# Kernel tuning notes

Hardware: AMD Instinct MI355X
Metric: run time of the kernel (lower is better)

The kernel has to match this reference:

```python
import jax, jax.numpy as jnp
import numpy as np

N_SITES = 64   # lattice sites
BOND = 32      # virtual bond dimension D
PHYS = 2       # physical (spin) dimension
BATCH = 32768  # Monte Carlo samples


def spin_to_occupancy(s):
    # spins in {-1,+1} -> physical indices in {0,1}
    return ((s + 1) // 2).astype(jnp.int32)


def setup_inputs() -> dict:
    key = jax.random.key(0)
    k1, k2, k3, k4 = jax.random.split(key, 4)
    # site tensors: boundary sites have bond dim 1, interior sites are (PHYS, D, D)
    t_first = jax.random.uniform(k1, (PHYS, 1, BOND), dtype=jnp.float32)
    t_mid = jax.random.uniform(k2, (N_SITES - 2, PHYS, BOND, BOND), dtype=jnp.float32)
    t_last = jax.random.uniform(k3, (PHYS, BOND, 1), dtype=jnp.float32)
    bits = jax.random.randint(k4, (BATCH, N_SITES), 0, 2)
    x = (2 * bits - 1).astype(jnp.int32)  # spins +-1
    return {"t_first": t_first, "t_mid": t_mid, "t_last": t_last, "x": x}


def reference(t_first, t_mid, t_last, x):
    idx = spin_to_occupancy(x)  # (B, n_sites)
    # first site: left bond = 1, so state = t_first[idx0, 0, :]  (B, D)
    state = t_first[idx[:, 0], 0, :]

    # interior sites: sequential chain of gather + batched mat-vec
    def step(state, xs):
        T, i = xs            # T: (PHYS, D, D), i: (B,)
        mats = T[i]          # (B, D, D) gather by physical index
        return jnp.einsum('bi,bij->bj', state, mats), None

    state, _ = jax.lax.scan(step, state, (t_mid, idx[:, 1:-1].T))

    # last site: right bond = 1
    amps = jnp.einsum('bi,bi->b', state, t_last[idx[:, -1], :, 0])  # (B,)
    return jnp.log(amps)
```

## Files before the change

### kernel.cpp

```cpp
#include <hip/hip_runtime.h>
#include <math.h>

#define N_MID 62
#define BATCH 32768

typedef float f32x4 __attribute__((ext_vector_type(4)));
typedef short s16x8 __attribute__((ext_vector_type(8)));
typedef unsigned int u32x4 __attribute__((ext_vector_type(4)));

__device__ __forceinline__ short f2bf(float f) {
    unsigned u = __float_as_uint(f);
    return (short)((u + 0x8000u) >> 16);
}

__global__ __launch_bounds__(64) void prefix_kernel(const float* __restrict__ t_mid,
                                                    short* __restrict__ wsA) {
    int f = blockIdx.x;
    int l = threadIdx.x;
    int t = f & 1, b = (f >> 1) & 1, s = f >> 2;
    int q = l >> 4, m = l & 15;
    const float* src = t_mid + (size_t)(s * 2 + b) * 1024;
    s16x8 v;
    #pragma unroll
    for (int j = 0; j < 8; ++j) {
        int lam = 16 * (j >> 2) + 4 * q + (j & 3);
        v[j] = f2bf(src[lam * 32 + 16 * t + m]);
    }
    ((s16x8*)wsA)[f * 64 + l] = v;
}

__global__ __launch_bounds__(256) void mps_mfma_kernel(
    const float* __restrict__ t_first,
    const float* __restrict__ t_last,
    const int*   __restrict__ x,
    const short* __restrict__ wsA,
    float* __restrict__ out)
{
    const int tid  = threadIdx.x;
    const int w    = tid >> 6;
    const int l    = tid & 63;
    const int q    = l >> 4;
    const int e    = l & 15;
    const int base = (blockIdx.x * 4 + w) * 16;

    unsigned long long mask;
    {
        const int4* xr = (const int4*)(x + (size_t)(base + e) * 64 + 16 * q);
        unsigned chunk = 0;
        #pragma unroll
        for (int c = 0; c < 4; ++c) {
            int4 v = xr[c];
            chunk |= (unsigned)(v.x > 0) << (4 * c + 0);
            chunk |= (unsigned)(v.y > 0) << (4 * c + 1);
            chunk |= (unsigned)(v.z > 0) << (4 * c + 2);
            chunk |= (unsigned)(v.w > 0) << (4 * c + 3);
        }
        unsigned sh = chunk << ((q & 1) * 16);
        unsigned lo = (q < 2) ? sh : 0u;
        unsigned hi = (q >= 2) ? sh : 0u;
        lo |= (unsigned)__shfl_xor((int)lo, 16);
        lo |= (unsigned)__shfl_xor((int)lo, 32);
        hi |= (unsigned)__shfl_xor((int)hi, 16);
        hi |= (unsigned)__shfl_xor((int)hi, 32);
        mask = ((unsigned long long)hi << 32) | lo;
    }

    float st[8];
    {
        const float* tf = t_first + ((mask & 1ull) ? 32 : 0);
        #pragma unroll
        for (int j = 0; j < 8; ++j)
            st[j] = tf[16 * (j >> 2) + 4 * q + (j & 3)];
    }
    unsigned long long mrot = mask >> 1;

    s16x8 Bst;
    {
        u32x4 bp;
        #pragma unroll
        for (int d = 0; d < 4; ++d)
            bp[d] = __builtin_amdgcn_perm(__float_as_uint(st[2 * d + 1]),
                                          __float_as_uint(st[2 * d]), 0x07060302u);
        Bst = __builtin_bit_cast(s16x8, bp);
    }

    int expsum = 0;
    const f32x4 cz = {0.f, 0.f, 0.f, 0.f};

    const s16x8* bpa = (const s16x8*)wsA + l;
    s16x8 A0[4], A1[4];
    #pragma unroll
    for (int f = 0; f < 4; ++f) A0[f] = bpa[f * 64];
    #pragma unroll
    for (int f = 0; f < 4; ++f) A1[f] = bpa[(4 + f) * 64];

    auto site = [&](s16x8* A, const s16x8* pf, bool resc) {
        f32x4 y00 = __builtin_amdgcn_mfma_f32_16x16x32_bf16(A[0], Bst, cz, 0, 0, 0);
        f32x4 y01 = __builtin_amdgcn_mfma_f32_16x16x32_bf16(A[1], Bst, cz, 0, 0, 0);
        f32x4 y10 = __builtin_amdgcn_mfma_f32_16x16x32_bf16(A[2], Bst, cz, 0, 0, 0);
        f32x4 y11 = __builtin_amdgcn_mfma_f32_16x16x32_bf16(A[3], Bst, cz, 0, 0, 0);

        if (pf) {
            #pragma unroll
            for (int f = 0; f < 4; ++f) A[f] = pf[f * 64];
        }

        bool hi = (mrot & 1ull) != 0;
        mrot >>= 1;
        #pragma unroll
        for (int r = 0; r < 4; ++r) {
            st[r]     = hi ? y10[r] : y00[r];
            st[4 + r] = hi ? y11[r] : y01[r];
        }

        if (resc) {
            float mx = st[0];
            #pragma unroll
            for (int j = 1; j < 8; ++j) mx = fmaxf(mx, st[j]);
            mx = fmaxf(mx, __shfl_xor(mx, 16));
            mx = fmaxf(mx, __shfl_xor(mx, 32));
            int ex = (int)((__float_as_uint(mx) >> 23) & 0xFF) - 127;
            float sc = __uint_as_float((unsigned)(127 - ex) << 23);
            #pragma unroll
            for (int j = 0; j < 8; ++j) st[j] *= sc;
            expsum += ex;
        }

        u32x4 bp;
        #pragma unroll
        for (int d = 0; d < 4; ++d)
            bp[d] = __builtin_amdgcn_perm(__float_as_uint(st[2 * d + 1]),
                                          __float_as_uint(st[2 * d]), 0x07060302u);
        Bst = __builtin_bit_cast(s16x8, bp);
    };

    const s16x8* pf = bpa + 8 * 64;
    for (int s2 = 0; s2 < 31; ++s2) {
        bool more = (s2 < 30);
        site(A0, more ? pf : nullptr, false);
        site(A1, more ? pf + 4 * 64 : nullptr, (s2 & 3) == 3);
        pf += 8 * 64;
    }

    const float* tl = t_last + ((mrot & 1ull) ? 32 : 0);
    float amp = 0.f;
    #pragma unroll
    for (int j = 0; j < 8; ++j)
        amp = fmaf(st[j], tl[16 * (j >> 2) + 4 * q + (j & 3)], amp);
    amp += __shfl_xor(amp, 16);
    amp += __shfl_xor(amp, 32);

    if (l < 16)
        out[base + l] = logf(amp) + 0.69314718055994531f * (float)expsum;
}

extern "C" void kernel_launch(void* const* d_in, const int* in_sizes, int n_in,
                              void* d_out, int out_size, void* d_ws, size_t ws_size,
                              hipStream_t stream) {
    const float* t_first = (const float*)d_in[0];
    const float* t_mid   = (const float*)d_in[1];
    const float* t_last  = (const float*)d_in[2];
    const int*   x       = (const int*)d_in[3];
    float* out           = (float*)d_out;

    short* wsA = (short*)d_ws;

    hipLaunchKernelGGL(prefix_kernel, dim3(N_MID * 4), dim3(64), 0, stream, t_mid, wsA);
    hipLaunchKernelGGL(mps_mfma_kernel, dim3(BATCH / 64), dim3(256), 0, stream,
                       t_first, t_last, x, wsA, out);
}
```

Measured before the change: 83.51 us.

## Process two 16-sample groups per wave to reuse site matrices and interleave MFMA chains

Each wave now carries two independent batch groups (32 samples) through the chain, issuing eight MFMAs per site that share the same loaded A fragments. Site matrices are prefetched four sites ahead instead of two. This halves weight loads per sample and gives the MFMA pipe two independent dependency chains, which hides the latency of the serial per-site recurrence. The cost is higher register pressure and half as many blocks, which reduces occupancy. The launch-bounds hint is set for this.

```diff
diff --git a/kernel.cpp b/kernel.cpp
--- a/kernel.cpp
+++ b/kernel.cpp
@@ -29,7 +29,7 @@
     ((s16x8*)wsA)[f * 64 + l] = v;
 }
 
-__global__ __launch_bounds__(256) void mps_mfma_kernel(
+__global__ __launch_bounds__(256, 1) void mps_mfma_kernel(
     const float* __restrict__ t_first,
     const float* __restrict__ t_last,
     const int*   __restrict__ x,
@@ -41,11 +41,10 @@
     const int l    = tid & 63;
     const int q    = l >> 4;
     const int e    = l & 15;
-    const int base = (blockIdx.x * 4 + w) * 16;
+    const int base = (blockIdx.x * 4 + w) * 32;
 
-    unsigned long long mask;
-    {
-        const int4* xr = (const int4*)(x + (size_t)(base + e) * 64 + 16 * q);
+    auto build_mask = [&](int elem) -> unsigned long long {
+        const int4* xr = (const int4*)(x + (size_t)elem * 64 + 16 * q);
         unsigned chunk = 0;
         #pragma unroll
         for (int c = 0; c < 4; ++c) {
@@ -62,96 +61,119 @@
         lo |= (unsigned)__shfl_xor((int)lo, 32);
         hi |= (unsigned)__shfl_xor((int)hi, 16);
         hi |= (unsigned)__shfl_xor((int)hi, 32);
-        mask = ((unsigned long long)hi << 32) | lo;
+        return ((unsigned long long)hi << 32) | lo;
+    };
+    unsigned long long mrotA = build_mask(base + e);
+    unsigned long long mrotB = build_mask(base + 16 + e);
+
+    float stA[8], stB[8];
+    {
+        const float* tfA = t_first + ((mrotA & 1ull) ? 32 : 0);
+        const float* tfB = t_first + ((mrotB & 1ull) ? 32 : 0);
+        #pragma unroll
+        for (int j = 0; j < 8; ++j) {
+            int c = 16 * (j >> 2) + 4 * q + (j & 3);
+            stA[j] = tfA[c];
+            stB[j] = tfB[c];
+        }
     }
+    mrotA >>= 1;
+    mrotB >>= 1;
 
-    float st[8];
-    {
-        const float* tf = t_first + ((mask & 1ull) ? 32 : 0);
-        #pragma unroll
-        for (int j = 0; j < 8; ++j)
-            st[j] = tf[16 * (j >> 2) + 4 * q + (j & 3)];
-    }
-    unsigned long long mrot = mask >> 1;
-
-    s16x8 Bst;
-    {
+    s16x8 BstA, BstB;
+    auto packB = [&](const float* st) -> s16x8 {
         u32x4 bp;
         #pragma unroll
         for (int d = 0; d < 4; ++d)
             bp[d] = __builtin_amdgcn_perm(__float_as_uint(st[2 * d + 1]),
                                           __float_as_uint(st[2 * d]), 0x07060302u);
-        Bst = __builtin_bit_cast(s16x8, bp);
-    }
+        return __builtin_bit_cast(s16x8, bp);
+    };
+    BstA = packB(stA);
+    BstB = packB(stB);
 
-    int expsum = 0;
+    int expA = 0, expB = 0;
     const f32x4 cz = {0.f, 0.f, 0.f, 0.f};
 
-    const s16x8* bpa = (const s16x8*)wsA + l;
-    s16x8 A0[4], A1[4];
+    const s16x8* pA = (const s16x8*)wsA + l;
+    s16x8 A[4][4];
     #pragma unroll
-    for (int f = 0; f < 4; ++f) A0[f] = bpa[f * 64];
-    #pragma unroll
-    for (int f = 0; f < 4; ++f) A1[f] = bpa[(4 + f) * 64];
+    for (int sl = 0; sl < 4; ++sl)
+        #pragma unroll
+        for (int f = 0; f < 4; ++f)
+            A[sl][f] = pA[(sl * 4 + f) * 64];
+    const s16x8* pp = pA + 16 * 64;
 
-    auto site = [&](s16x8* A, const s16x8* pf, bool resc) {
-        f32x4 y00 = __builtin_amdgcn_mfma_f32_16x16x32_bf16(A[0], Bst, cz, 0, 0, 0);
-        f32x4 y01 = __builtin_amdgcn_mfma_f32_16x16x32_bf16(A[1], Bst, cz, 0, 0, 0);
-        f32x4 y10 = __builtin_amdgcn_mfma_f32_16x16x32_bf16(A[2], Bst, cz, 0, 0, 0);
-        f32x4 y11 = __builtin_amdgcn_mfma_f32_16x16x32_bf16(A[3], Bst, cz, 0, 0, 0);
+    auto site = [&](s16x8* A4, const s16x8* pf, bool resc) {
+        f32x4 ya00 = __builtin_amdgcn_mfma_f32_16x16x32_bf16(A4[0], BstA, cz, 0, 0, 0);
+        f32x4 ya01 = __builtin_amdgcn_mfma_f32_16x16x32_bf16(A4[1], BstA, cz, 0, 0, 0);
+        f32x4 ya10 = __builtin_amdgcn_mfma_f32_16x16x32_bf16(A4[2], BstA, cz, 0, 0, 0);
+        f32x4 ya11 = __builtin_amdgcn_mfma_f32_16x16x32_bf16(A4[3], BstA, cz, 0, 0, 0);
+        f32x4 yb00 = __builtin_amdgcn_mfma_f32_16x16x32_bf16(A4[0], BstB, cz, 0, 0, 0);
+        f32x4 yb01 = __builtin_amdgcn_mfma_f32_16x16x32_bf16(A4[1], BstB, cz, 0, 0, 0);
+        f32x4 yb10 = __builtin_amdgcn_mfma_f32_16x16x32_bf16(A4[2], BstB, cz, 0, 0, 0);
+        f32x4 yb11 = __builtin_amdgcn_mfma_f32_16x16x32_bf16(A4[3], BstB, cz, 0, 0, 0);
 
         if (pf) {
             #pragma unroll
-            for (int f = 0; f < 4; ++f) A[f] = pf[f * 64];
+            for (int f = 0; f < 4; ++f) A4[f] = pf[f * 64];
         }
 
-        bool hi = (mrot & 1ull) != 0;
-        mrot >>= 1;
+        bool hiA = (mrotA & 1ull) != 0; mrotA >>= 1;
+        bool hiB = (mrotB & 1ull) != 0; mrotB >>= 1;
         #pragma unroll
         for (int r = 0; r < 4; ++r) {
-            st[r]     = hi ? y10[r] : y00[r];
-            st[4 + r] = hi ? y11[r] : y01[r];
+            stA[r]     = hiA ? ya10[r] : ya00[r];
+            stA[4 + r] = hiA ? ya11[r] : ya01[r];
+            stB[r]     = hiB ? yb10[r] : yb00[r];
+            stB[4 + r] = hiB ? yb11[r] : yb01[r];
         }
 
         if (resc) {
-            float mx = st[0];
+            float mxA = stA[0], mxB = stB[0];
             #pragma unroll
-            for (int j = 1; j < 8; ++j) mx = fmaxf(mx, st[j]);
-            mx = fmaxf(mx, __shfl_xor(mx, 16));
-            mx = fmaxf(mx, __shfl_xor(mx, 32));
-            int ex = (int)((__float_as_uint(mx) >> 23) & 0xFF) - 127;
-            float sc = __uint_as_float((unsigned)(127 - ex) << 23);
+            for (int j = 1; j < 8; ++j) { mxA = fmaxf(mxA, stA[j]); mxB = fmaxf(mxB, stB[j]); }
+            mxA = fmaxf(mxA, __shfl_xor(mxA, 16)); mxA = fmaxf(mxA, __shfl_xor(mxA, 32));
+            mxB = fmaxf(mxB, __shfl_xor(mxB, 16)); mxB = fmaxf(mxB, __shfl_xor(mxB, 32));
+            int exA = (int)((__float_as_uint(mxA) >> 23) & 0xFF) - 127;
+            int exB = (int)((__float_as_uint(mxB) >> 23) & 0xFF) - 127;
+            float scA = __uint_as_float((unsigned)(127 - exA) << 23);
+            float scB = __uint_as_float((unsigned)(127 - exB) << 23);
             #pragma unroll
-            for (int j = 0; j < 8; ++j) st[j] *= sc;
-            expsum += ex;
+            for (int j = 0; j < 8; ++j) { stA[j] *= scA; stB[j] *= scB; }
+            expA += exA; expB += exB;
         }
 
-        u32x4 bp;
-        #pragma unroll
-        for (int d = 0; d < 4; ++d)
-            bp[d] = __builtin_amdgcn_perm(__float_as_uint(st[2 * d + 1]),
-                                          __float_as_uint(st[2 * d]), 0x07060302u);
-        Bst = __builtin_bit_cast(s16x8, bp);
+        BstA = packB(stA);
+        BstB = packB(stB);
     };
 
-    const s16x8* pf = bpa + 8 * 64;
-    for (int s2 = 0; s2 < 31; ++s2) {
-        bool more = (s2 < 30);
-        site(A0, more ? pf : nullptr, false);
-        site(A1, more ? pf + 4 * 64 : nullptr, (s2 & 3) == 3);
-        pf += 8 * 64;
+    for (int k = 0; k < 15; ++k) {
+        #pragma unroll
+        for (int sl = 0; sl < 4; ++sl) {
+            site(A[sl], pp, (sl == 3) && (k & 1));
+            pp += 4 * 64;
+        }
     }
+    site(A[0], nullptr, false);
+    site(A[1], nullptr, false);
 
-    const float* tl = t_last + ((mrot & 1ull) ? 32 : 0);
-    float amp = 0.f;
+    const float* tlA = t_last + ((mrotA & 1ull) ? 32 : 0);
+    const float* tlB = t_last + ((mrotB & 1ull) ? 32 : 0);
+    float ampA = 0.f, ampB = 0.f;
     #pragma unroll
-    for (int j = 0; j < 8; ++j)
-        amp = fmaf(st[j], tl[16 * (j >> 2) + 4 * q + (j & 3)], amp);
-    amp += __shfl_xor(amp, 16);
-    amp += __shfl_xor(amp, 32);
+    for (int j = 0; j < 8; ++j) {
+        int c = 16 * (j >> 2) + 4 * q + (j & 3);
+        ampA = fmaf(stA[j], tlA[c], ampA);
+        ampB = fmaf(stB[j], tlB[c], ampB);
+    }
+    ampA += __shfl_xor(ampA, 16); ampA += __shfl_xor(ampA, 32);
+    ampB += __shfl_xor(ampB, 16); ampB += __shfl_xor(ampB, 32);
 
-    if (l < 16)
-        out[base + l] = logf(amp) + 0.69314718055994531f * (float)expsum;
+    if (l < 16) {
+        out[base + l]      = logf(ampA) + 0.69314718055994531f * (float)expA;
+        out[base + 16 + l] = logf(ampB) + 0.69314718055994531f * (float)expB;
+    }
 }
 
 extern "C" void kernel_launch(void* const* d_in, const int* in_sizes, int n_in,
@@ -166,6 +188,6 @@
     short* wsA = (short*)d_ws;
 
     hipLaunchKernelGGL(prefix_kernel, dim3(N_MID * 4), dim3(64), 0, stream, t_mid, wsA);
-    hipLaunchKernelGGL(mps_mfma_kernel, dim3(BATCH / 64), dim3(256), 0, stream,
+    hipLaunchKernelGGL(mps_mfma_kernel, dim3(BATCH / 128), dim3(256), 0, stream,
                        t_first, t_last, x, wsA, out);
 }
```

After: 85.59 us. 2.5% more time.

## Precompute pairwise site products in FP8 and select via masked MFMA

Applied to the files above, without the earlier changes.

The prefix kernel now multiplies adjacent pairs of site matrices for all four physical-index combinations and stores the products as FP8. This halves the sequential chain length from 62 to 31 steps. The main loop uses FP8 MFMAs and selects the right product by zeroing the B operand for the three unused combinations, with a rescale after every step. This removes dependent steps from the latency-bound chain but quadruples MFMA count per step, and FP8 on both the matrices and the state risks large accuracy loss.

```diff
diff --git a/kernel.cpp b/kernel.cpp
--- a/kernel.cpp
+++ b/kernel.cpp
@@ -2,38 +2,73 @@
 #include <math.h>
 
 #define N_MID 62
+#define NPAIR 31
 #define BATCH 32768
 
 typedef float f32x4 __attribute__((ext_vector_type(4)));
-typedef short s16x8 __attribute__((ext_vector_type(8)));
+typedef unsigned int u32x2 __attribute__((ext_vector_type(2)));
 typedef unsigned int u32x4 __attribute__((ext_vector_type(4)));
 
-__device__ __forceinline__ short f2bf(float f) {
-    unsigned u = __float_as_uint(f);
-    return (short)((u + 0x8000u) >> 16);
+__device__ __forceinline__ long mklong(unsigned a, unsigned b) {
+    u32x2 t = {a, b};
+    return __builtin_bit_cast(long, t);
+}
+__device__ __forceinline__ unsigned pack_fp8x4(float a, float b, float c, float d) {
+    int r = __builtin_amdgcn_cvt_pk_fp8_f32(a, b, 0, false);
+    r = __builtin_amdgcn_cvt_pk_fp8_f32(c, d, r, true);
+    return (unsigned)r;
 }
 
 __global__ __launch_bounds__(64) void prefix_kernel(const float* __restrict__ t_mid,
-                                                    short* __restrict__ wsA) {
-    int f = blockIdx.x;
-    int l = threadIdx.x;
-    int t = f & 1, b = (f >> 1) & 1, s = f >> 2;
-    int q = l >> 4, m = l & 15;
-    const float* src = t_mid + (size_t)(s * 2 + b) * 1024;
-    s16x8 v;
+                                                    unsigned* __restrict__ wsP) {
+    __shared__ float M1s[1024], M2s[1024];
+    const int l = threadIdx.x, q = l >> 4, m = l & 15;
+    const int i = blockIdx.x >> 2, v = blockIdx.x & 3;
+
+    const float4* s1 = (const float4*)(t_mid + (size_t)((2 * i) * 2 + (v & 1)) * 1024);
+    const float4* s2 = (const float4*)(t_mid + (size_t)((2 * i + 1) * 2 + (v >> 1)) * 1024);
+    #pragma unroll
+    for (int c = 0; c < 4; ++c) {
+        ((float4*)M1s)[c * 64 + l] = s1[c * 64 + l];
+        ((float4*)M2s)[c * 64 + l] = s2[c * 64 + l];
+    }
+    __syncthreads();
+
+    float colv[2][32];
+    #pragma unroll
+    for (int t = 0; t < 2; ++t)
+        #pragma unroll
+        for (int mm = 0; mm < 32; ++mm)
+            colv[t][mm] = M2s[mm * 32 + 16 * t + m];
+
+    float o0[8], o1[8];
     #pragma unroll
     for (int j = 0; j < 8; ++j) {
-        int lam = 16 * (j >> 2) + 4 * q + (j & 3);
-        v[j] = f2bf(src[lam * 32 + 16 * t + m]);
+        int a = 16 * (j >> 2) + 4 * q + (j & 3);
+        float acc0 = 0.f, acc1 = 0.f;
+        #pragma unroll
+        for (int mm = 0; mm < 32; ++mm) {
+            float r = M1s[a * 32 + mm];
+            acc0 = fmaf(r, colv[0][mm], acc0);
+            acc1 = fmaf(r, colv[1][mm], acc1);
+        }
+        o0[j] = acc0;
+        o1[j] = acc1;
     }
-    ((s16x8*)wsA)[f * 64 + l] = v;
+
+    u32x4 outw;
+    outw[0] = pack_fp8x4(o0[0], o0[1], o0[2], o0[3]);
+    outw[1] = pack_fp8x4(o0[4], o0[5], o0[6], o0[7]);
+    outw[2] = pack_fp8x4(o1[0], o1[1], o1[2], o1[3]);
+    outw[3] = pack_fp8x4(o1[4], o1[5], o1[6], o1[7]);
+    ((u32x4*)wsP)[blockIdx.x * 64 + l] = outw;
 }
 
-__global__ __launch_bounds__(256) void mps_mfma_kernel(
+__global__ __launch_bounds__(256, 2) void mps_mfma_kernel(
     const float* __restrict__ t_first,
     const float* __restrict__ t_last,
     const int*   __restrict__ x,
-    const short* __restrict__ wsA,
+    const unsigned* __restrict__ wsP,
     float* __restrict__ out)
 {
     const int tid  = threadIdx.x;
@@ -43,17 +78,17 @@
     const int e    = l & 15;
     const int base = (blockIdx.x * 4 + w) * 16;
 
-    unsigned long long mask;
+    unsigned long long mrot;
     {
         const int4* xr = (const int4*)(x + (size_t)(base + e) * 64 + 16 * q);
         unsigned chunk = 0;
         #pragma unroll
         for (int c = 0; c < 4; ++c) {
-            int4 v = xr[c];
-            chunk |= (unsigned)(v.x > 0) << (4 * c + 0);
-            chunk |= (unsigned)(v.y > 0) << (4 * c + 1);
-            chunk |= (unsigned)(v.z > 0) << (4 * c + 2);
-            chunk |= (unsigned)(v.w > 0) << (4 * c + 3);
+            int4 vv = xr[c];
+            chunk |= (unsigned)(vv.x > 0) << (4 * c + 0);
+            chunk |= (unsigned)(vv.y > 0) << (4 * c + 1);
+            chunk |= (unsigned)(vv.z > 0) << (4 * c + 2);
+            chunk |= (unsigned)(vv.w > 0) << (4 * c + 3);
         }
         unsigned sh = chunk << ((q & 1) * 16);
         unsigned lo = (q < 2) ? sh : 0u;
@@ -62,85 +97,77 @@
         lo |= (unsigned)__shfl_xor((int)lo, 32);
         hi |= (unsigned)__shfl_xor((int)hi, 16);
         hi |= (unsigned)__shfl_xor((int)hi, 32);
-        mask = ((unsigned long long)hi << 32) | lo;
+        unsigned long long mask = ((unsigned long long)hi << 32) | lo;
+        const float* tf = t_first + ((mask & 1ull) ? 32 : 0);
+        mrot = mask >> 1;
+        (void)tf;
     }
 
     float st[8];
     {
-        const float* tf = t_first + ((mask & 1ull) ? 32 : 0);
+        const float* tf = t_first + ((x[(size_t)(base + e) * 64] > 0) ? 32 : 0);
         #pragma unroll
         for (int j = 0; j < 8; ++j)
             st[j] = tf[16 * (j >> 2) + 4 * q + (j & 3)];
     }
-    unsigned long long mrot = mask >> 1;
-
-    s16x8 Bst;
-    {
-        u32x4 bp;
-        #pragma unroll
-        for (int d = 0; d < 4; ++d)
-            bp[d] = __builtin_amdgcn_perm(__float_as_uint(st[2 * d + 1]),
-                                          __float_as_uint(st[2 * d]), 0x07060302u);
-        Bst = __builtin_bit_cast(s16x8, bp);
-    }
+    unsigned Bd0 = pack_fp8x4(st[0], st[1], st[2], st[3]);
+    unsigned Bd1 = pack_fp8x4(st[4], st[5], st[6], st[7]);
 
     int expsum = 0;
     const f32x4 cz = {0.f, 0.f, 0.f, 0.f};
 
-    const s16x8* bpa = (const s16x8*)wsA + l;
-    s16x8 A0[4], A1[4];
+    const u32x4* W = (const u32x4*)wsP + l;
+    u32x4 Q0[4], Q1[4];
     #pragma unroll
-    for (int f = 0; f < 4; ++f) A0[f] = bpa[f * 64];
+    for (int v = 0; v < 4; ++v) Q0[v] = W[v * 64];
     #pragma unroll
-    for (int f = 0; f < 4; ++f) A1[f] = bpa[(4 + f) * 64];
+    for (int v = 0; v < 4; ++v) Q1[v] = W[(4 + v) * 64];
 
-    auto site = [&](s16x8* A, const s16x8* pf, bool resc) {
-        f32x4 y00 = __builtin_amdgcn_mfma_f32_16x16x32_bf16(A[0], Bst, cz, 0, 0, 0);
-        f32x4 y01 = __builtin_amdgcn_mfma_f32_16x16x32_bf16(A[1], Bst, cz, 0, 0, 0);
-        f32x4 y10 = __builtin_amdgcn_mfma_f32_16x16x32_bf16(A[2], Bst, cz, 0, 0, 0);
-        f32x4 y11 = __builtin_amdgcn_mfma_f32_16x16x32_bf16(A[3], Bst, cz, 0, 0, 0);
+    auto step = [&](u32x4* Q, const u32x4* pf) {
+        unsigned vl = (unsigned)mrot & 3u;
+        mrot >>= 2;
+
+        f32x4 y0 = cz, y1 = cz;
+        #pragma unroll
+        for (int v = 0; v < 4; ++v) {
+            long A0 = mklong(Q[v][0], Q[v][1]);
+            long A1 = mklong(Q[v][2], Q[v][3]);
+            bool sel = (vl == (unsigned)v);
+            long u = mklong(sel ? Bd0 : 0u, sel ? Bd1 : 0u);
+            y0 = __builtin_amdgcn_mfma_f32_16x16x32_fp8_fp8(A0, u, y0, 0, 0, 0);
+            y1 = __builtin_amdgcn_mfma_f32_16x16x32_fp8_fp8(A1, u, y1, 0, 0, 0);
+        }
 
         if (pf) {
             #pragma unroll
-            for (int f = 0; f < 4; ++f) A[f] = pf[f * 64];
+            for (int v = 0; v < 4; ++v) Q[v] = pf[v * 64];
         }
 
-        bool hi = (mrot & 1ull) != 0;
-        mrot >>= 1;
         #pragma unroll
-        for (int r = 0; r < 4; ++r) {
-            st[r]     = hi ? y10[r] : y00[r];
-            st[4 + r] = hi ? y11[r] : y01[r];
-        }
+        for (int r = 0; r < 4; ++r) { st[r] = y0[r]; st[4 + r] = y1[r]; }
 
-        if (resc) {
-            float mx = st[0];
-            #pragma unroll
-            for (int j = 1; j < 8; ++j) mx = fmaxf(mx, st[j]);
-            mx = fmaxf(mx, __shfl_xor(mx, 16));
-            mx = fmaxf(mx, __shfl_xor(mx, 32));
-            int ex = (int)((__float_as_uint(mx) >> 23) & 0xFF) - 127;
-            float sc = __uint_as_float((unsigned)(127 - ex) << 23);
-            #pragma unroll
-            for (int j = 0; j < 8; ++j) st[j] *= sc;
-            expsum += ex;
-        }
+        float mx = st[0];
+        #pragma unroll
+        for (int j = 1; j < 8; ++j) mx = fmaxf(mx, st[j]);
+        mx = fmaxf(mx, __shfl_xor(mx, 16));
+        mx = fmaxf(mx, __shfl_xor(mx, 32));
+        int ex = (int)((__float_as_uint(mx) >> 23) & 0xFF) - 127;
+        float sc = __uint_as_float((unsigned)(127 - ex) << 23);
+        #pragma unroll
+        for (int j = 0; j < 8; ++j) st[j] *= sc;
+        expsum += ex;
 
-        u32x4 bp;
-        #pragma unroll
-        for (int d = 0; d < 4; ++d)
-            bp[d] = __builtin_amdgcn_perm(__float_as_uint(st[2 * d + 1]),
-                                          __float_as_uint(st[2 * d]), 0x07060302u);
-        Bst = __builtin_bit_cast(s16x8, bp);
+        Bd0 = pack_fp8x4(st[0], st[1], st[2], st[3]);
+        Bd1 = pack_fp8x4(st[4], st[5], st[6], st[7]);
     };
 
-    const s16x8* pf = bpa + 8 * 64;
-    for (int s2 = 0; s2 < 31; ++s2) {
-        bool more = (s2 < 30);
-        site(A0, more ? pf : nullptr, false);
-        site(A1, more ? pf + 4 * 64 : nullptr, (s2 & 3) == 3);
+    const u32x4* pf = W + 8 * 64;
+    for (int k = 0; k < 15; ++k) {
+        step(Q0, pf);
+        step(Q1, (k < 14) ? pf + 4 * 64 : nullptr);
         pf += 8 * 64;
     }
+    step(Q0, nullptr);
 
     const float* tl = t_last + ((mrot & 1ull) ? 32 : 0);
     float amp = 0.f;
@@ -163,9 +190,9 @@
     const int*   x       = (const int*)d_in[3];
     float* out           = (float*)d_out;
 
-    short* wsA = (short*)d_ws;
+    unsigned* wsP = (unsigned*)d_ws;
 
-    hipLaunchKernelGGL(prefix_kernel, dim3(N_MID * 4), dim3(64), 0, stream, t_mid, wsA);
+    hipLaunchKernelGGL(prefix_kernel, dim3(NPAIR * 4), dim3(64), 0, stream, t_mid, wsP);
     hipLaunchKernelGGL(mps_mfma_kernel, dim3(BATCH / 64), dim3(256), 0, stream,
-                       t_first, t_last, x, wsA, out);
+                       t_first, t_last, x, wsP, out);
 }
```

Result: faster. 77.70 us (-7.0%).
